# Kernel tuning notes

Hardware: AMD Instinct MI355X
Metric: run time of the kernel (lower is better)

The kernel has to match this reference:

```python
import jax, jax.numpy as jnp
import numpy as np

ALPHA = 0.1  # GCN2Conv alpha; theta=None => beta=1.0 so out = ((1-a)*prop + a*x0) @ W


def gcn_norm(edge_index, n):
    # PyG gcn_norm with add_self_loops=True and unit edge weights.
    row, col = edge_index[0], edge_index[1]
    loop = jnp.arange(n, dtype=edge_index.dtype)
    row = jnp.concatenate([row, loop])
    col = jnp.concatenate([col, loop])
    w = jnp.ones(row.shape[0], dtype=jnp.float32)
    deg = jax.ops.segment_sum(w, col, num_segments=n)
    dis = jnp.where(deg > 0, jax.lax.rsqrt(jnp.maximum(deg, 1e-12)), 0.0)
    norm = dis[row] * w * dis[col]
    return row, col, norm


def propagate(x, row, col, norm, n):
    # out[col] += norm * x[row]  (source->target aggregation)
    return jax.ops.segment_sum(x[row] * norm[:, None], col, num_segments=n)


def setup_inputs() -> dict:
    key = jax.random.key(0)
    ks = jax.random.split(key, 6)
    N, E, F, L = 100000, 1000000, 64, 4
    x = jax.random.normal(ks[0], (N, F), dtype=jnp.float32)
    edge_index = jax.random.randint(ks[1], (2, E), 0, N, dtype=jnp.int64)
    gcn2_w = jax.random.normal(ks[2], (L, F, F), dtype=jnp.float32) * (1.0 / np.sqrt(F))
    w1 = jax.random.normal(ks[3], (F, 16), dtype=jnp.float32) * (1.0 / np.sqrt(F))
    b1 = jnp.zeros((16,), dtype=jnp.float32)
    w2 = jax.random.normal(ks[4], (16, 1), dtype=jnp.float32) * (1.0 / np.sqrt(16))
    b2 = jnp.zeros((1,), dtype=jnp.float32)
    return {"x": x, "edge_index": edge_index, "gcn2_w": gcn2_w,
            "w1": w1, "b1": b1, "w2": w2, "b2": b2}


def reference(x, edge_index, gcn2_w, w1, b1, w2, b2):
    n = x.shape[0]
    row, col, norm = gcn_norm(edge_index, n)
    x0 = x
    h = x
    # GCN2Conv stack: h = relu(((1-a)*Ah + a*x0) @ W)
    for l in range(gcn2_w.shape[0]):
        p = propagate(h, row, col, norm, n)
        h = jax.nn.relu(((1.0 - ALPHA) * p + ALPHA * x0) @ gcn2_w[l])
    # GCNConv(F,16): lin -> propagate -> bias
    h = propagate(h @ w1, row, col, norm, n) + b1
    # GCNConv(16,1)
    h = propagate(h @ w2, row, col, norm, n) + b2
    return jax.nn.sigmoid(h).squeeze(1).astype(jnp.float32)
```

## Files before the change

kernel.cpp:

```cpp
#include <hip/hip_runtime.h>
#include <hip/hip_fp16.h>
#include <math.h>

#define ALPHA 0.1f
#define CHUNK 8192

typedef _Float16 f16x8 __attribute__((ext_vector_type(8)));
typedef float f32x4 __attribute__((ext_vector_type(4)));


__global__ void k_zero(int* a, int n) {
    int i = blockIdx.x * blockDim.x + threadIdx.x;
    if (i < n) a[i] = 0;
}

__global__ __launch_bounds__(256) void kb_hist(const int* __restrict__ col, int e,
                                               int nbuck, int* __restrict__ tot) {
    __shared__ int h[1024];
    int t = threadIdx.x;
    for (int i = t; i < 1024; i += 256) h[i] = 0;
    __syncthreads();
    int base = blockIdx.x * CHUNK;
    int end = min(base + CHUNK, e);
    for (int i = base + t; i < end; i += 256)
        atomicAdd(&h[col[i] >> 7], 1);
    __syncthreads();
    for (int i = t; i < nbuck; i += 256)
        if (h[i]) atomicAdd(&tot[i], h[i]);
}

__global__ __launch_bounds__(1024) void kb_scan(const int* __restrict__ tot,
                                                int* __restrict__ start,
                                                int* __restrict__ cursor, int nbuck) {
    __shared__ int s[1024];
    int t = threadIdx.x;
    int v = (t < nbuck) ? tot[t] : 0;
    s[t] = v;
    __syncthreads();
    for (int d = 1; d < 1024; d <<= 1) {
        int add = (t >= d) ? s[t - d] : 0;
        __syncthreads();
        s[t] += add;
        __syncthreads();
    }
    if (t < nbuck) { start[t] = s[t] - v; cursor[t] = s[t] - v; }
    if (t == nbuck - 1) start[nbuck] = s[t];
}

__global__ __launch_bounds__(256) void kb_part(const int* __restrict__ row,
                                               const int* __restrict__ col,
                                               int e, int nbuck,
                                               int* __restrict__ cursor,
                                               int* __restrict__ part) {
    __shared__ int lcnt[1024];
    __shared__ int lbase[1024];
    int t = threadIdx.x;
    for (int i = t; i < 1024; i += 256) lcnt[i] = 0;
    __syncthreads();
    int base = blockIdx.x * CHUNK;
    int end = min(base + CHUNK, e);
    for (int i = base + t; i < end; i += 256)
        atomicAdd(&lcnt[col[i] >> 7], 1);
    __syncthreads();
    for (int i = t; i < nbuck; i += 256) {
        int c = lcnt[i];
        lbase[i] = c ? atomicAdd(&cursor[i], c) : 0;
    }
    __syncthreads();
    for (int i = t; i < 1024; i += 256) lcnt[i] = 0;
    __syncthreads();
    for (int i = base + t; i < end; i += 256) {
        int cl = col[i];
        int b = cl >> 7;
        int lp = atomicAdd(&lcnt[b], 1);
        part[lbase[b] + lp] = ((cl & 127) << 17) | row[i];
    }
}

__global__ __launch_bounds__(256) void kb_csr(const int* __restrict__ start,
                                              const int* __restrict__ part, int n,
                                              float* __restrict__ dis,
                                              int* __restrict__ off,
                                              int* __restrict__ srow) {
    __shared__ int cnt[128], excl[128], stmp[128];
    int b = blockIdx.x;
    int t = threadIdx.x;
    int bstart = start[b], bend = start[b + 1];
    if (t < 128) cnt[t] = 0;
    __syncthreads();
    for (int i = bstart + t; i < bend; i += 256)
        atomicAdd(&cnt[part[i] >> 17], 1);
    __syncthreads();
    if (t < 128) stmp[t] = cnt[t];
    __syncthreads();
    for (int d = 1; d < 128; d <<= 1) {
        int add = (t < 128 && t >= d) ? stmp[t - d] : 0;
        __syncthreads();
        if (t < 128) stmp[t] += add;
        __syncthreads();
    }
    if (t < 128) {
        excl[t] = stmp[t] - cnt[t];
        int c = (b << 7) + t;
        if (c < n) {
            off[c] = bstart + stmp[t];
            dis[c] = rsqrtf((float)cnt[t] + 1.0f);
        }
        cnt[t] = 0;
    }
    __syncthreads();
    for (int i = bstart + t; i < bend; i += 256) {
        int pk = part[i];
        int cl = pk >> 17;
        int lp = atomicAdd(&cnt[cl], 1);
        srow[bstart + excl[cl] + lp] = pk & 0x1FFFF;
    }
}

__global__ void k_prescale(const float* __restrict__ x, const float* __restrict__ dis,
                           __half* __restrict__ xs, __half* __restrict__ x0h,
                           long long total) {
    long long i = (long long)blockIdx.x * blockDim.x + threadIdx.x;
    if (i >= total) return;
    float xv = x[i];
    float d = dis[i >> 6];
    xs[i] = __float2half(d * xv);
    x0h[i] = __float2half(ALPHA * xv);
}


__global__ __launch_bounds__(256) void k_gcn2_fused(
    const int* __restrict__ srow, const int* __restrict__ endoff,
    const float* __restrict__ dis, const __half* __restrict__ hs_in,
    const __half* __restrict__ x0h, const float* __restrict__ W,
    __half* __restrict__ hs_out, int n)
{
    __shared__ __half WsT[64][72];
    __shared__ __half vs[32][72];
    __shared__ float dcs[32];

    int t = threadIdx.x;
    int w = t >> 6;
    int lane = t & 63;
    int nb = blockIdx.x * 32;

    for (int i = t; i < 4096; i += 256) {
        int k = i >> 6, nf = i & 63;
        WsT[nf][k] = __float2half(W[i]);
    }

    int j = lane >> 3;
    int s = lane & 7;
    int local = w * 8 + j;
    int c = nb + local;
    bool valid = c < n;
    int cc = valid ? c : 0;
    int start = (cc == 0) ? 0 : endoff[cc - 1];
    int end = valid ? endoff[cc] : 0;
    float dc = dis[cc];

    float a0, a1, a2, a3, a4, a5, a6, a7;
    {
        f16x8 q = *(const f16x8*)(hs_in + (size_t)cc * 64 + s * 8);
        a0 = (float)q[0]; a1 = (float)q[1]; a2 = (float)q[2]; a3 = (float)q[3];
        a4 = (float)q[4]; a5 = (float)q[5]; a6 = (float)q[6]; a7 = (float)q[7];
    }
    for (int e = start; e < end; e++) {
        int r = srow[e];
        f16x8 q = *(const f16x8*)(hs_in + (size_t)r * 64 + s * 8);
        a0 += (float)q[0]; a1 += (float)q[1]; a2 += (float)q[2]; a3 += (float)q[3];
        a4 += (float)q[4]; a5 += (float)q[5]; a6 += (float)q[6]; a7 += (float)q[7];
    }
    if (valid) {
        float dc9 = (1.0f - ALPHA) * dc;
        f16x8 xv = *(const f16x8*)(x0h + (size_t)cc * 64 + s * 8);
        f16x8 vv;
        vv[0] = (_Float16)(dc9 * a0 + (float)xv[0]);
        vv[1] = (_Float16)(dc9 * a1 + (float)xv[1]);
        vv[2] = (_Float16)(dc9 * a2 + (float)xv[2]);
        vv[3] = (_Float16)(dc9 * a3 + (float)xv[3]);
        vv[4] = (_Float16)(dc9 * a4 + (float)xv[4]);
        vv[5] = (_Float16)(dc9 * a5 + (float)xv[5]);
        vv[6] = (_Float16)(dc9 * a6 + (float)xv[6]);
        vv[7] = (_Float16)(dc9 * a7 + (float)xv[7]);
        *(f16x8*)&vs[local][s * 8] = vv;
        if (s == 0) dcs[local] = dc;
    }
    __syncthreads();

    int m16 = lane & 15;
    int quad = lane >> 4;
#pragma unroll
    for (int mt = 0; mt < 2; mt++) {
        f32x4 acc = {0.0f, 0.0f, 0.0f, 0.0f};
#pragma unroll
        for (int kk = 0; kk < 64; kk += 32) {
            f16x8 af = *(const f16x8*)&vs[mt * 16 + m16][kk + quad * 8];
            f16x8 bf = *(const f16x8*)&WsT[w * 16 + m16][kk + quad * 8];
            acc = __builtin_amdgcn_mfma_f32_16x16x32_f16(af, bf, acc, 0, 0, 0);
        }
#pragma unroll
        for (int r = 0; r < 4; r++) {
            int loc = mt * 16 + quad * 4 + r;
            int cn = nb + loc;
            if (cn < n) {
                float h = fmaxf(acc[r], 0.0f);
                hs_out[(size_t)cn * 64 + w * 16 + m16] = __float2half(dcs[loc] * h);
            }
        }
    }
}


__global__ __launch_bounds__(256) void k_lin1(const __half* __restrict__ hs,
                                              const float* __restrict__ w1,
                                              __half* __restrict__ t16s, int n) {
    __shared__ float Ws[64 * 16];
    int t = threadIdx.x;
    for (int i = t; i < 64 * 16; i += 256) Ws[i] = w1[i];
    __syncthreads();
    long long idx = (long long)blockIdx.x * 256 + t;
    int r = (int)(idx >> 4), j = (int)(idx & 15);
    if (r >= n) return;
    const __half* hp = hs + (size_t)r * 64;
    float acc = 0.0f;
#pragma unroll
    for (int k = 0; k < 64; k += 2) {
        float2 u = __half22float2(*(const __half2*)(hp + k));
        acc = fmaf(u.x, Ws[k * 16 + j], acc);
        acc = fmaf(u.y, Ws[(k + 1) * 16 + j], acc);
    }
    t16s[idx] = __float2half(acc);
}


__global__ __launch_bounds__(256) void k_prop16_lin2(
    const int* __restrict__ srow, const int* __restrict__ endoff,
    const float* __restrict__ dis, const __half* __restrict__ t16s,
    const float* __restrict__ b1, const float* __restrict__ w2,
    float* __restrict__ t1s, int n)
{
    int t = threadIdx.x;
    int w = t >> 6, lane = t & 63;
    int g = lane >> 2;
    int s = lane & 3;
    int c = blockIdx.x * 4 + w;
    if (c >= n) return;
    int start = (c == 0) ? 0 : endoff[c - 1];
    int end = endoff[c];
    float a0 = 0, a1 = 0, a2 = 0, a3 = 0;
    if (g == 0) {
        float2 q = *(const float2*)(t16s + (size_t)c * 16 + s * 4);
        float2 u;
        u = __half22float2(*(__half2*)&q.x); a0 = u.x; a1 = u.y;
        u = __half22float2(*(__half2*)&q.y); a2 = u.x; a3 = u.y;
    }
    for (int e = start + g; e < end; e += 16) {
        int r = srow[e];
        float2 q = *(const float2*)(t16s + (size_t)r * 16 + s * 4);
        float2 u;
        u = __half22float2(*(__half2*)&q.x); a0 += u.x; a1 += u.y;
        u = __half22float2(*(__half2*)&q.y); a2 += u.x; a3 += u.y;
    }
#pragma unroll
    for (int d = 4; d <= 32; d <<= 1) {
        a0 += __shfl_xor(a0, d, 64); a1 += __shfl_xor(a1, d, 64);
        a2 += __shfl_xor(a2, d, 64); a3 += __shfl_xor(a3, d, 64);
    }
    float dc = dis[c];
    float4 b = *(const float4*)(b1 + s * 4);
    float4 ww = *(const float4*)(w2 + s * 4);
    float partial = (dc * a0 + b.x) * ww.x + (dc * a1 + b.y) * ww.y +
                    (dc * a2 + b.z) * ww.z + (dc * a3 + b.w) * ww.w;
    partial += __shfl_xor(partial, 1, 64);
    partial += __shfl_xor(partial, 2, 64);
    if (lane == 0) t1s[c] = dc * partial;
}


__global__ void k_prop1(const int* __restrict__ srow, const int* __restrict__ endoff,
                        const float* __restrict__ dis, const float* __restrict__ t1s,
                        const float* __restrict__ b2, float* __restrict__ out, int n) {
    int c = blockIdx.x * blockDim.x + threadIdx.x;
    if (c >= n) return;
    int start = (c == 0) ? 0 : endoff[c - 1];
    int end = endoff[c];
    float ssum = t1s[c];
    for (int e = start; e < end; e++) ssum += t1s[srow[e]];
    float v = dis[c] * ssum + b2[0];
    out[c] = 1.0f / (1.0f + expf(-v));
}


static inline char* align16(char* p) {
    return (char*)(((uintptr_t)p + 15) & ~(uintptr_t)15);
}

extern "C" void kernel_launch(void* const* d_in, const int* in_sizes, int n_in,
                              void* d_out, int out_size, void* d_ws, size_t ws_size,
                              hipStream_t stream) {
    const float* x  = (const float*)d_in[0];
    const int*   ei = (const int*)d_in[1];
    const float* gw = (const float*)d_in[2];
    const float* w1 = (const float*)d_in[3];
    const float* b1 = (const float*)d_in[4];
    const float* w2 = (const float*)d_in[5];
    const float* b2 = (const float*)d_in[6];
    float* out = (float*)d_out;

    const int N = in_sizes[0] / 64;
    const int E = in_sizes[1] / 2;
    const int L = in_sizes[2] / (64 * 64);

    const int* row = ei;
    const int* col = ei + E;

    const int NB = (N + 127) >> 7;

    char* p = (char*)d_ws;
    int* off = (int*)p;            p = align16(p + (size_t)N * 4);
    float* dis = (float*)p;        p = align16(p + (size_t)N * 4);
    int* srow = (int*)p;           p = align16(p + (size_t)E * 4);
    int* bstart = (int*)p;         p = align16(p + (size_t)(NB + 1) * 4);
    int* bcur = (int*)p;           p = align16(p + (size_t)NB * 4);
    int* btot = (int*)p;           p = align16(p + (size_t)NB * 4);
    __half* hsA = (__half*)p;      p = align16(p + (size_t)N * 128);
    __half* hsB = (__half*)p;      p = align16(p + (size_t)N * 128);
    __half* x0h = (__half*)p;      p = align16(p + (size_t)N * 128);
    __half* t16s = (__half*)p;     p = align16(p + (size_t)N * 32);
    float* t1s = (float*)p;
    int* part = (int*)hsB;

    const int B = 256;
    int gN = (N + B - 1) / B;
    int gPart = (E + CHUNK - 1) / CHUNK;

    k_zero<<<(NB + B - 1) / B, B, 0, stream>>>(btot, NB);
    kb_hist<<<gPart, B, 0, stream>>>(col, E, NB, btot);
    kb_scan<<<1, 1024, 0, stream>>>(btot, bstart, bcur, NB);
    kb_part<<<gPart, B, 0, stream>>>(row, col, E, NB, bcur, part);
    kb_csr<<<NB, B, 0, stream>>>(bstart, part, N, dis, off, srow);

    long long tot64 = (long long)N * 64;
    k_prescale<<<(int)((tot64 + B - 1) / B), B, 0, stream>>>(x, dis, hsA, x0h, tot64);

    __half* bufs[2] = {hsA, hsB};
    const __half* hin = hsA;
    for (int l = 0; l < L; l++) {
        __half* hout = bufs[(l + 1) & 1];
        k_gcn2_fused<<<(N + 31) / 32, B, 0, stream>>>(srow, off, dis, hin, x0h,
                                                      gw + (long long)l * 64 * 64, hout, N);
        hin = hout;
    }

    k_lin1<<<(int)(((long long)N * 16 + B - 1) / B), B, 0, stream>>>(hin, w1, t16s, N);
    k_prop16_lin2<<<(N + 3) / 4, B, 0, stream>>>(srow, off, dis, t16s, b1, w2, t1s, N);
    k_prop1<<<gN, B, 0, stream>>>(srow, off, dis, t1s, b2, out, N);
}
```

Measured before the change: 354.4 us.

## Fuse prescale into CSR build, lin1 into last GCN2 layer, pretranspose weights

```diff
diff --git a/kernel.cpp b/kernel.cpp
--- a/kernel.cpp
+++ b/kernel.cpp
@@ -79,10 +79,14 @@
 
 __global__ __launch_bounds__(256) void kb_csr(const int* __restrict__ start,
                                               const int* __restrict__ part, int n,
+                                              const float* __restrict__ x,
                                               float* __restrict__ dis,
                                               int* __restrict__ off,
-                                              int* __restrict__ srow) {
+                                              int* __restrict__ srow,
+                                              __half* __restrict__ xs,
+                                              __half* __restrict__ x0h) {
     __shared__ int cnt[128], excl[128], stmp[128];
+    __shared__ float disl[128];
     int b = blockIdx.x;
     int t = threadIdx.x;
     int bstart = start[b], bend = start[b + 1];
@@ -102,9 +106,11 @@
     if (t < 128) {
         excl[t] = stmp[t] - cnt[t];
         int c = (b << 7) + t;
+        float d = rsqrtf((float)cnt[t] + 1.0f);
+        disl[t] = d;
         if (c < n) {
             off[c] = bstart + stmp[t];
-            dis[c] = rsqrtf((float)cnt[t] + 1.0f);
+            dis[c] = d;
         }
         cnt[t] = 0;
     }
@@ -115,39 +121,50 @@
         int lp = atomicAdd(&cnt[cl], 1);
         srow[bstart + excl[cl] + lp] = pk & 0x1FFFF;
     }
-}
-
-__global__ void k_prescale(const float* __restrict__ x, const float* __restrict__ dis,
-                           __half* __restrict__ xs, __half* __restrict__ x0h,
-                           long long total) {
-    long long i = (long long)blockIdx.x * blockDim.x + threadIdx.x;
-    if (i >= total) return;
-    float xv = x[i];
-    float d = dis[i >> 6];
-    xs[i] = __float2half(d * xv);
-    x0h[i] = __float2half(ALPHA * xv);
+    int c0 = b << 7;
+    for (int i = t; i < 128 * 64; i += 256) {
+        int node = c0 + (i >> 6);
+        if (node >= n) break;
+        float xv = x[(size_t)node * 64 + (i & 63)];
+        float d = disl[i >> 6];
+        xs[(size_t)node * 64 + (i & 63)] = __float2half(d * xv);
+        x0h[(size_t)node * 64 + (i & 63)] = __float2half(ALPHA * xv);
+    }
+}
+
+
+__global__ void k_prep(const float* __restrict__ gw, const float* __restrict__ w1,
+                       __half* __restrict__ whT, __half* __restrict__ w1T, int L) {
+    int i = blockIdx.x * blockDim.x + threadIdx.x;
+    int tot = L * 4096;
+    if (i < tot) {
+        int l = i >> 12, r = i & 4095;
+        int k = r >> 6, nf = r & 63;
+        whT[(l << 12) + nf * 64 + k] = __float2half(gw[i]);
+    } else if (i < tot + 1024) {
+        int r = i - tot;
+        int k = r >> 4, nf = r & 15;
+        w1T[nf * 64 + k] = __float2half(w1[r]);
+    }
 }
 
 
 __global__ __launch_bounds__(256) void k_gcn2_fused(
     const int* __restrict__ srow, const int* __restrict__ endoff,
     const float* __restrict__ dis, const __half* __restrict__ hs_in,
-    const __half* __restrict__ x0h, const float* __restrict__ W,
-    __half* __restrict__ hs_out, int n)
+    const __half* __restrict__ x0h, const __half* __restrict__ whT,
+    __half* __restrict__ hs_out,
+    const __half* __restrict__ w1T,
+    __half* __restrict__ t16s, int n)
 {
-    __shared__ __half WsT[64][72];
     __shared__ __half vs[32][72];
+    __shared__ __half vs2[32][72];
     __shared__ float dcs[32];
 
     int t = threadIdx.x;
     int w = t >> 6;
     int lane = t & 63;
     int nb = blockIdx.x * 32;
-
-    for (int i = t; i < 4096; i += 256) {
-        int k = i >> 6, nf = i & 63;
-        WsT[nf][k] = __float2half(W[i]);
-    }
 
     int j = lane >> 3;
     int s = lane & 7;
@@ -160,20 +177,36 @@
     float dc = dis[cc];
 
     float a0, a1, a2, a3, a4, a5, a6, a7;
+    float b0 = 0, b1 = 0, b2 = 0, b3 = 0, b4 = 0, b5 = 0, b6 = 0, b7 = 0;
     {
         f16x8 q = *(const f16x8*)(hs_in + (size_t)cc * 64 + s * 8);
         a0 = (float)q[0]; a1 = (float)q[1]; a2 = (float)q[2]; a3 = (float)q[3];
         a4 = (float)q[4]; a5 = (float)q[5]; a6 = (float)q[6]; a7 = (float)q[7];
     }
-    for (int e = start; e < end; e++) {
-        int r = srow[e];
-        f16x8 q = *(const f16x8*)(hs_in + (size_t)r * 64 + s * 8);
-        a0 += (float)q[0]; a1 += (float)q[1]; a2 += (float)q[2]; a3 += (float)q[3];
-        a4 += (float)q[4]; a5 += (float)q[5]; a6 += (float)q[6]; a7 += (float)q[7];
-    }
+    int e = start;
+    for (; e + 2 <= end; e += 2) {
+        int r0 = srow[e];
+        int r1 = srow[e + 1];
+        f16x8 q0 = *(const f16x8*)(hs_in + (size_t)r0 * 64 + s * 8);
+        f16x8 q1 = *(const f16x8*)(hs_in + (size_t)r1 * 64 + s * 8);
+        a0 += (float)q0[0]; a1 += (float)q0[1]; a2 += (float)q0[2]; a3 += (float)q0[3];
+        a4 += (float)q0[4]; a5 += (float)q0[5]; a6 += (float)q0[6]; a7 += (float)q0[7];
+        b0 += (float)q1[0]; b1 += (float)q1[1]; b2 += (float)q1[2]; b3 += (float)q1[3];
+        b4 += (float)q1[4]; b5 += (float)q1[5]; b6 += (float)q1[6]; b7 += (float)q1[7];
+    }
+    if (e < end) {
+        int r0 = srow[e];
+        f16x8 q0 = *(const f16x8*)(hs_in + (size_t)r0 * 64 + s * 8);
+        a0 += (float)q0[0]; a1 += (float)q0[1]; a2 += (float)q0[2]; a3 += (float)q0[3];
+        a4 += (float)q0[4]; a5 += (float)q0[5]; a6 += (float)q0[6]; a7 += (float)q0[7];
+    }
+    a0 += b0; a1 += b1; a2 += b2; a3 += b3;
+    a4 += b4; a5 += b5; a6 += b6; a7 += b7;
+
     if (valid) {
         float dc9 = (1.0f - ALPHA) * dc;
-        f16x8 xv = *(const f16x8*)(x0h + (size_t)cc * 64 + s * 8);
+        const f16x8* xp = (const f16x8*)(x0h + (size_t)cc * 64 + s * 8);
+        f16x8 xv = __builtin_nontemporal_load(xp);
         f16x8 vv;
         vv[0] = (_Float16)(dc9 * a0 + (float)xv[0]);
         vv[1] = (_Float16)(dc9 * a1 + (float)xv[1]);
@@ -190,47 +223,54 @@
 
     int m16 = lane & 15;
     int quad = lane >> 4;
+    f16x8 bf0 = *(const f16x8*)(whT + (size_t)(w * 16 + m16) * 64 + quad * 8);
+    f16x8 bf1 = *(const f16x8*)(whT + (size_t)(w * 16 + m16) * 64 + 32 + quad * 8);
+    bool last = (w1T != nullptr);
 #pragma unroll
     for (int mt = 0; mt < 2; mt++) {
         f32x4 acc = {0.0f, 0.0f, 0.0f, 0.0f};
+        f16x8 af0 = *(const f16x8*)&vs[mt * 16 + m16][quad * 8];
+        f16x8 af1 = *(const f16x8*)&vs[mt * 16 + m16][32 + quad * 8];
+        acc = __builtin_amdgcn_mfma_f32_16x16x32_f16(af0, bf0, acc, 0, 0, 0);
+        acc = __builtin_amdgcn_mfma_f32_16x16x32_f16(af1, bf1, acc, 0, 0, 0);
+        if (!last) {
 #pragma unroll
-        for (int kk = 0; kk < 64; kk += 32) {
-            f16x8 af = *(const f16x8*)&vs[mt * 16 + m16][kk + quad * 8];
-            f16x8 bf = *(const f16x8*)&WsT[w * 16 + m16][kk + quad * 8];
-            acc = __builtin_amdgcn_mfma_f32_16x16x32_f16(af, bf, acc, 0, 0, 0);
-        }
+            for (int r = 0; r < 4; r++) {
+                int loc = mt * 16 + quad * 4 + r;
+                int cn = nb + loc;
+                if (cn < n) {
+                    float h = fmaxf(acc[r], 0.0f);
+                    hs_out[(size_t)cn * 64 + w * 16 + m16] = __float2half(dcs[loc] * h);
+                }
+            }
+        } else {
 #pragma unroll
-        for (int r = 0; r < 4; r++) {
-            int loc = mt * 16 + quad * 4 + r;
-            int cn = nb + loc;
-            if (cn < n) {
-                float h = fmaxf(acc[r], 0.0f);
-                hs_out[(size_t)cn * 64 + w * 16 + m16] = __float2half(dcs[loc] * h);
+            for (int r = 0; r < 4; r++) {
+                int loc = mt * 16 + quad * 4 + r;
+                vs2[loc][w * 16 + m16] = __float2half(fmaxf(acc[r], 0.0f));
             }
         }
     }
-}
-
-
-__global__ __launch_bounds__(256) void k_lin1(const __half* __restrict__ hs,
-                                              const float* __restrict__ w1,
-                                              __half* __restrict__ t16s, int n) {
-    __shared__ float Ws[64 * 16];
-    int t = threadIdx.x;
-    for (int i = t; i < 64 * 16; i += 256) Ws[i] = w1[i];
-    __syncthreads();
-    long long idx = (long long)blockIdx.x * 256 + t;
-    int r = (int)(idx >> 4), j = (int)(idx & 15);
-    if (r >= n) return;
-    const __half* hp = hs + (size_t)r * 64;
-    float acc = 0.0f;
+
+    if (last) {
+        __syncthreads();
+        if (w < 2) {
+            f16x8 c0 = *(const f16x8*)(w1T + (size_t)m16 * 64 + quad * 8);
+            f16x8 c1 = *(const f16x8*)(w1T + (size_t)m16 * 64 + 32 + quad * 8);
+            f16x8 af0 = *(const f16x8*)&vs2[w * 16 + m16][quad * 8];
+            f16x8 af1 = *(const f16x8*)&vs2[w * 16 + m16][32 + quad * 8];
+            f32x4 acc = {0.0f, 0.0f, 0.0f, 0.0f};
+            acc = __builtin_amdgcn_mfma_f32_16x16x32_f16(af0, c0, acc, 0, 0, 0);
+            acc = __builtin_amdgcn_mfma_f32_16x16x32_f16(af1, c1, acc, 0, 0, 0);
 #pragma unroll
-    for (int k = 0; k < 64; k += 2) {
-        float2 u = __half22float2(*(const __half2*)(hp + k));
-        acc = fmaf(u.x, Ws[k * 16 + j], acc);
-        acc = fmaf(u.y, Ws[(k + 1) * 16 + j], acc);
-    }
-    t16s[idx] = __float2half(acc);
+            for (int r = 0; r < 4; r++) {
+                int loc = w * 16 + quad * 4 + r;
+                int cn = nb + loc;
+                if (cn < n)
+                    t16s[(size_t)cn * 16 + m16] = __float2half(dcs[loc] * acc[r]);
+            }
+        }
+    }
 }
 
 
@@ -324,6 +364,8 @@
     int* bstart = (int*)p;         p = align16(p + (size_t)(NB + 1) * 4);
     int* bcur = (int*)p;           p = align16(p + (size_t)NB * 4);
     int* btot = (int*)p;           p = align16(p + (size_t)NB * 4);
+    __half* whT = (__half*)p;      p = align16(p + (size_t)L * 4096 * 2);
+    __half* w1T = (__half*)p;      p = align16(p + 1024 * 2);
     __half* hsA = (__half*)p;      p = align16(p + (size_t)N * 128);
     __half* hsB = (__half*)p;      p = align16(p + (size_t)N * 128);
     __half* x0h = (__half*)p;      p = align16(p + (size_t)N * 128);
@@ -335,25 +377,25 @@
     int gN = (N + B - 1) / B;
     int gPart = (E + CHUNK - 1) / CHUNK;
 
+    k_prep<<<(L * 4096 + 1024 + B - 1) / B, B, 0, stream>>>(gw, w1, whT, w1T, L);
+
     k_zero<<<(NB + B - 1) / B, B, 0, stream>>>(btot, NB);
     kb_hist<<<gPart, B, 0, stream>>>(col, E, NB, btot);
     kb_scan<<<1, 1024, 0, stream>>>(btot, bstart, bcur, NB);
     kb_part<<<gPart, B, 0, stream>>>(row, col, E, NB, bcur, part);
-    kb_csr<<<NB, B, 0, stream>>>(bstart, part, N, dis, off, srow);
-
-    long long tot64 = (long long)N * 64;
-    k_prescale<<<(int)((tot64 + B - 1) / B), B, 0, stream>>>(x, dis, hsA, x0h, tot64);
+    kb_csr<<<NB, B, 0, stream>>>(bstart, part, N, x, dis, off, srow, hsA, x0h);
 
     __half* bufs[2] = {hsA, hsB};
     const __half* hin = hsA;
     for (int l = 0; l < L; l++) {
-        __half* hout = bufs[(l + 1) & 1];
-        k_gcn2_fused<<<(N + 31) / 32, B, 0, stream>>>(srow, off, dis, hin, x0h,
-                                                      gw + (long long)l * 64 * 64, hout, N);
+        bool lastl = (l == L - 1);
+        __half* hout = lastl ? nullptr : bufs[(l + 1) & 1];
+        k_gcn2_fused<<<(N + 31) / 32, B, 0, stream>>>(
+            srow, off, dis, hin, x0h, whT + (size_t)l * 4096,
+            hout, lastl ? w1T : nullptr, t16s, N);
         hin = hout;
     }
 
-    k_lin1<<<(int)(((long long)N * 16 + B - 1) / B), B, 0, stream>>>(hin, w1, t16s, N);
     k_prop16_lin2<<<(N + 3) / 4, B, 0, stream>>>(srow, off, dis, t16s, b1, w2, t1s, N);
     k_prop1<<<gN, B, 0, stream>>>(srow, off, dis, t1s, b2, out, N);
 }
```

Result: faster. 338.7 us (-4.4%).
